# Kernel optimization log

Hardware: AMD Instinct MI355X
Metric: run time of the kernel (lower is better)

The kernel has to match this reference:

```python
import jax, jax.numpy as jnp
import numpy as np

N = 100000
E = 3200000
F_IN = 128
H = 64
B = 128


def _sage(x, edge_index, Wl, bl, Wr):
    # PyG SAGEConv (aggr='mean'): out = lin_l(mean_{j in N(i)} x_j) + lin_r(x_i)
    src, dst = edge_index[0], edge_index[1]
    msg = x[src]                                            # [E, F] gather
    agg = jax.ops.segment_sum(msg, dst, num_segments=x.shape[0])
    cnt = jax.ops.segment_sum(jnp.ones((edge_index.shape[1],), x.dtype), dst,
                              num_segments=x.shape[0])
    mean = agg / jnp.maximum(cnt, 1.0)[:, None]
    return mean @ Wl + bl + x @ Wr


def _encode(x, edge_index, batch, p1, p2, num_graphs):
    h = jax.nn.relu(_sage(x, edge_index, *p1))
    h = jax.nn.relu(_sage(h, edge_index, *p2))
    # global_mean_pool
    s = jax.ops.segment_sum(h, batch, num_segments=num_graphs)
    c = jax.ops.segment_sum(jnp.ones((h.shape[0],), h.dtype), batch,
                            num_segments=num_graphs)
    return s / jnp.maximum(c, 1.0)[:, None]


def setup_inputs() -> dict:
    key = jax.random.key(0)
    ks = jax.random.split(key, 20)
    inp = {
        "state_x": jax.random.normal(ks[0], (N, F_IN), dtype=jnp.float32),
        "state_edge_index": jax.random.randint(ks[1], (2, E), 0, N),
        "state_batch": jnp.sort(jax.random.randint(ks[2], (N,), 0, B)),
        "goal_x": jax.random.normal(ks[3], (N, F_IN), dtype=jnp.float32),
        "goal_edge_index": jax.random.randint(ks[4], (2, E), 0, N),
        "goal_batch": jnp.sort(jax.random.randint(ks[5], (N,), 0, B)),
        "depth": jax.random.uniform(ks[6], (B, 1), dtype=jnp.float32) * 20.0,
    }
    def lin(k, fin, fout):
        s = 1.0 / np.sqrt(fin)
        return jax.random.uniform(k, (fin, fout), minval=-s, maxval=s, dtype=jnp.float32)
    # SAGEConv params: Wl (neighbor, with bias), Wr (root, no bias)
    names = ["s1", "s2", "g1", "g2"]
    fins = [F_IN, H, F_IN, H]
    for i, (nm, fin) in enumerate(zip(names, fins)):
        inp[nm + "_Wl"] = lin(ks[7 + 3 * i], fin, H)
        inp[nm + "_bl"] = jnp.zeros((H,), jnp.float32)
        inp[nm + "_Wr"] = lin(ks[8 + 3 * i], fin, H)
    inp["mlp_W1"] = lin(ks[19], 2 * H + 1, H)
    inp["mlp_b1"] = jnp.zeros((H,), jnp.float32)
    inp["mlp_W2"] = lin(jax.random.fold_in(key, 99), H, 1)
    inp["mlp_b2"] = jnp.zeros((1,), jnp.float32)
    return inp


def reference(state_x, state_edge_index, state_batch,
              goal_x, goal_edge_index, goal_batch, depth,
              s1_Wl, s1_bl, s1_Wr, s2_Wl, s2_bl, s2_Wr,
              g1_Wl, g1_bl, g1_Wr, g2_Wl, g2_bl, g2_Wr,
              mlp_W1, mlp_b1, mlp_W2, mlp_b2):
    state_emb = _encode(state_x, state_edge_index, state_batch,
                        (s1_Wl, s1_bl, s1_Wr), (s2_Wl, s2_bl, s2_Wr), B)
    goal_emb = _encode(goal_x, goal_edge_index, goal_batch,
                       (g1_Wl, g1_bl, g1_Wr), (g2_Wl, g2_bl, g2_Wr), B)
    graph_emb = jnp.concatenate([state_emb, goal_emb], axis=1)   # [B, 2H]
    d_mean = depth.mean()
    d_std = depth.std()  # unbiased=False matches jnp default
    d = (depth - d_mean) / (d_std + 1e-6)
    features = jnp.concatenate([graph_emb, d], axis=1)           # [B, 2H+1]
    h = jax.nn.relu(features @ mlp_W1 + mlp_b1)
    out = h @ mlp_W2 + mlp_b2                                    # [B, 1]
    return out[:, 0]
```

## Files before the change

### kernel.cpp

```cpp
#include <hip/hip_runtime.h>
#include <hip/hip_bf16.h>
#include <hip/hip_fp16.h>


#define NB    128
#define EPB   16384
#define BWMAX 1024
#define PP    8
#define SRCB  17
#define SCAP  28672

typedef _Float16 v2h __attribute__((ext_vector_type(2)));
union U2H { unsigned int u; v2h h; __half2 hh; };

static __device__ __forceinline__ unsigned int pack2(float a, float b) {
    U2H t; t.hh = __floats2half2_rn(a, b); return t.u;
}
static __device__ __forceinline__ float dot2(unsigned int x, unsigned int w, float acc) {
    U2H xa, wa; xa.u = x; wa.u = w;
    return __builtin_amdgcn_fdot2(xa.h, wa.h, acc, false);
}


__global__ __launch_bounds__(256) void p1_hist(const int* __restrict__ dstS,
                                               const int* __restrict__ dstG,
                                               int* __restrict__ blkhist,
                                               int E, int bsh, int nblk) {
    const int g = blockIdx.x / nblk;
    const int blk = blockIdx.x % nblk;
    const int* __restrict__ dst = g ? dstG : dstS;
    __shared__ int h[NB];
    for (int i = threadIdx.x; i < NB; i += 256) h[i] = 0;
    __syncthreads();
    const int base = blk * EPB;
    for (int k = 0; k < EPB; k += 256) {
        const int e = base + k + threadIdx.x;
        if (e < E) atomicAdd(&h[dst[e] >> bsh], 1);
    }
    __syncthreads();
    for (int i = threadIdx.x; i < NB; i += 256)
        blkhist[((size_t)(g * nblk + blk)) * NB + i] = h[i];
}

__global__ __launch_bounds__(NB) void p1_scan(const int* __restrict__ blkhist,
                                              int* __restrict__ basem,
                                              int* __restrict__ bucket_base,
                                              int nblk) {
    __shared__ int lds[NB];
    const int g = blockIdx.x;
    const int* __restrict__ bh = blkhist + (size_t)g * nblk * NB;
    int* __restrict__ bm = basem + (size_t)g * nblk * NB;
    int* __restrict__ bb = bucket_base + (size_t)g * (NB + 1);
    const int b = threadIdx.x;
    int s = 0;
    int k = 0;
    for (; k + 8 <= nblk; k += 8) {
        int v[8];
        #pragma unroll
        for (int t = 0; t < 8; ++t) v[t] = bh[(size_t)(k + t) * NB + b];
        #pragma unroll
        for (int t = 0; t < 8; ++t) s += v[t];
    }
    for (; k < nblk; ++k) s += bh[(size_t)k * NB + b];
    lds[b] = s;
    __syncthreads();
    for (int off = 1; off < NB; off <<= 1) {
        int v = (b >= off) ? lds[b - off] : 0;
        __syncthreads();
        lds[b] += v;
        __syncthreads();
    }
    int run = lds[b] - s;
    bb[b] = run;
    if (b == NB - 1) bb[NB] = run + s;
    k = 0;
    for (; k + 8 <= nblk; k += 8) {
        int c[8];
        #pragma unroll
        for (int t = 0; t < 8; ++t) c[t] = bh[(size_t)(k + t) * NB + b];
        #pragma unroll
        for (int t = 0; t < 8; ++t) {
            bm[(size_t)(k + t) * NB + b] = run;
            run += c[t];
        }
    }
    for (; k < nblk; ++k) {
        const int c = bh[(size_t)k * NB + b];
        bm[(size_t)k * NB + b] = run;
        run += c;
    }
}

__global__ __launch_bounds__(256) void p1_scatter(const int* __restrict__ eiS,
                                                  const int* __restrict__ eiG,
                                                  const int* __restrict__ basem,
                                                  int* __restrict__ pairs,
                                                  int E, int bsh, int nblk) {
    const int g = blockIdx.x / nblk;
    const int blk = blockIdx.x % nblk;
    const int* __restrict__ src = g ? eiG : eiS;
    const int* __restrict__ dst = src + E;
    int* __restrict__ pr = pairs + (size_t)g * E;
    const int bwm = (1 << bsh) - 1;
    __shared__ int cur[NB];
    for (int i = threadIdx.x; i < NB; i += 256)
        cur[i] = basem[((size_t)(g * nblk + blk)) * NB + i];
    __syncthreads();
    const int base = blk * EPB;
    for (int k = 0; k < EPB; k += 256) {
        const int e = base + k + threadIdx.x;
        if (e < E) {
            const int d = dst[e];
            const int s = src[e];
            const int p = atomicAdd(&cur[d >> bsh], 1);
            pr[p] = s | ((d & bwm) << SRCB);
        }
    }
}

__global__ __launch_bounds__(512) void p2_sort(const int* __restrict__ pairs,
                                               const int* __restrict__ bucket_base,
                                               int* __restrict__ csr,
                                               int* __restrict__ row_start,
                                               int N, int E, int bsh) {
    __shared__ int stage[SCAP];
    __shared__ int cnt[BWMAX];
    __shared__ int off[BWMAX];
    __shared__ int ws[512];
    const int g = blockIdx.x / NB;
    const int b = blockIdx.x % NB;
    const int bw = 1 << bsh;
    const int lo = b * bw;
    int nn = N - lo;
    if (nn <= 0) return;
    if (nn > bw) nn = bw;
    const int* __restrict__ pr = pairs + (size_t)g * E;
    const int* __restrict__ bb = bucket_base + (size_t)g * (NB + 1);
    int* __restrict__ cs = csr + (size_t)g * E;
    int* __restrict__ rs = row_start + (size_t)g * (N + 1);
    const int tid = threadIdx.x;
    for (int i = tid; i < nn; i += 512) cnt[i] = 0;
    __syncthreads();
    const int e0 = bb[b];
    const int e1 = bb[b + 1];
    const int ne = e1 - e0;
    for (int e = e0 + tid; e < e1; e += 512)
        atomicAdd(&cnt[pr[e] >> SRCB], 1);
    __syncthreads();
    {
        const int i0 = 2 * tid, i1 = 2 * tid + 1;
        const int c0 = (i0 < nn) ? cnt[i0] : 0;
        const int c1 = (i1 < nn) ? cnt[i1] : 0;
        const int s = c0 + c1;
        ws[tid] = s;
        __syncthreads();
        for (int o = 1; o < 512; o <<= 1) {
            int v = (tid >= o) ? ws[tid - o] : 0;
            __syncthreads();
            ws[tid] += v;
            __syncthreads();
        }
        const int base = e0 + ws[tid] - s;
        if (i0 < nn) off[i0] = base;
        if (i1 < nn) off[i1] = base + c0;
    }
    __syncthreads();
    for (int i = tid; i < nn; i += 512) {
        rs[lo + i] = off[i];
        cnt[i] = off[i];
    }
    if (lo + nn == N && tid == 0) rs[N] = e1;
    __syncthreads();
    if (ne <= SCAP) {
        for (int e = e0 + tid; e < e1; e += 512) {
            const int v = pr[e];
            const int pos = atomicAdd(&cnt[v >> SRCB], 1);
            stage[pos - e0] = v & ((1 << SRCB) - 1);
        }
        __syncthreads();
        for (int i = tid; i < ne; i += 512) cs[e0 + i] = stage[i];
    } else {
        for (int e = e0 + tid; e < e1; e += 512) {
            const int v = pr[e];
            const int pos = atomicAdd(&cnt[v >> SRCB], 1);
            cs[pos] = v & ((1 << SRCB) - 1);
        }
    }
}

template <int K>
__global__ __launch_bounds__(512) void gemm_fused(const float* __restrict__ x,
                                                  const float* __restrict__ Wl,
                                                  const float* __restrict__ Wr,
                                                  __hip_bfloat16* __restrict__ Y,
                                                  __hip_bfloat16* __restrict__ R, int n) {
    constexpr int KC = 64;
    constexpr int ROWS = 64;
    __shared__ uint4 ldsW4[(KC / 4) * 64];
    __shared__ unsigned int ldsXu[ROWS * (KC / 2)];
    const int tid = threadIdx.x;
    const int lane = tid & 63;
    const int wid = tid >> 6;
    const int rbase = blockIdx.x * ROWS;

    float accY[8], accR[8];
    #pragma unroll
    for (int r = 0; r < 8; ++r) { accY[r] = 0.f; accR[r] = 0.f; }

    for (int k0 = 0; k0 < K; k0 += KC) {
        __syncthreads();
        for (int i = tid; i < (KC / 4) * 64; i += 512) {
            const int gp = i >> 6;
            const int c = i & 63;
            const int ka = k0 + gp * 4;
            const float wl0 = Wl[(size_t)ka * 64 + c],       wr0 = Wr[(size_t)ka * 64 + c];
            const float wl1 = Wl[(size_t)(ka + 1) * 64 + c], wr1 = Wr[(size_t)(ka + 1) * 64 + c];
            const float wl2 = Wl[(size_t)(ka + 2) * 64 + c], wr2 = Wr[(size_t)(ka + 2) * 64 + c];
            const float wl3 = Wl[(size_t)(ka + 3) * 64 + c], wr3 = Wr[(size_t)(ka + 3) * 64 + c];
            ldsW4[i] = make_uint4(pack2(wl0, wl1), pack2(wr0, wr1),
                                  pack2(wl2, wl3), pack2(wr2, wr3));
        }
        {
            constexpr int F4R = KC / 4;
            for (int i = tid; i < ROWS * F4R; i += 512) {
                const int rr = i / F4R;
                const int cc = i % F4R;
                int row = rbase + rr;
                if (row > n - 1) row = n - 1;
                const float4 xv = *(const float4*)(x + (size_t)row * K + k0 + cc * 4);
                ldsXu[rr * (KC / 2) + cc * 2 + 0] = pack2(xv.x, xv.y);
                ldsXu[rr * (KC / 2) + cc * 2 + 1] = pack2(xv.z, xv.w);
            }
        }
        __syncthreads();
        const int rw = wid * 8;
        #pragma unroll 2
        for (int k8 = 0; k8 < KC / 8; ++k8) {
            const uint4 w0 = ldsW4[(k8 * 2 + 0) * 64 + lane];
            const uint4 w1 = ldsW4[(k8 * 2 + 1) * 64 + lane];
            #pragma unroll
            for (int r = 0; r < 8; ++r) {
                const uint4 xq = *(const uint4*)(&ldsXu[(rw + r) * (KC / 2) + k8 * 4]);
                float yv = accY[r];
                float zv = accR[r];
                yv = dot2(xq.x, w0.x, yv);
                zv = dot2(xq.x, w0.y, zv);
                yv = dot2(xq.y, w0.z, yv);
                zv = dot2(xq.y, w0.w, zv);
                yv = dot2(xq.z, w1.x, yv);
                zv = dot2(xq.z, w1.y, zv);
                yv = dot2(xq.w, w1.z, yv);
                zv = dot2(xq.w, w1.w, zv);
                accY[r] = yv;
                accR[r] = zv;
            }
        }
    }
    #pragma unroll
    for (int r = 0; r < 8; ++r) {
        const int row = rbase + wid * 8 + r;
        if (row < n) {
            Y[(size_t)row * 64 + lane] = __float2bfloat16(accY[r]);
            R[(size_t)row * 64 + lane] = __float2bfloat16(accR[r]);
        }
    }
}

__global__ __launch_bounds__(256) void agg_fused(const __hip_bfloat16* __restrict__ Y,
                                                 const __hip_bfloat16* __restrict__ R,
                                                 const float* __restrict__ bl,
                                                 const int* __restrict__ csr,
                                                 const int* __restrict__ row_start,
                                                 float* __restrict__ H, int n) {
    const int wid = threadIdx.x >> 6;
    const int lane = threadIdx.x & 63;
    const int i = blockIdx.x * 4 + wid;
    if (i >= n) return;
    const int r0 = __builtin_amdgcn_readfirstlane(row_start[i]);
    const int r1 = __builtin_amdgcn_readfirstlane(row_start[i + 1]);
    float a[32];
    #pragma unroll
    for (int t = 0; t < 32; ++t) a[t] = 0.f;
    int e = r0;
    for (; e + 32 <= r1; e += 32) {
        #pragma unroll
        for (int t = 0; t < 32; ++t)
            a[t] += __bfloat162float(Y[(size_t)csr[e + t] * 64 + lane]);
    }
    for (; e + 8 <= r1; e += 8) {
        #pragma unroll
        for (int t = 0; t < 8; ++t)
            a[t] += __bfloat162float(Y[(size_t)csr[e + t] * 64 + lane]);
    }
    for (; e < r1; ++e) a[0] += __bfloat162float(Y[(size_t)csr[e] * 64 + lane]);
    float acc = 0.f;
    #pragma unroll
    for (int t = 0; t < 32; ++t) acc += a[t];
    const int c = r1 - r0;
    const float sc = (c > 0) ? (1.0f / (float)c) : 1.0f;
    const float v = acc * sc + bl[lane] + __bfloat162float(R[(size_t)i * 64 + lane]);
    H[(size_t)i * 64 + lane] = fmaxf(v, 0.0f);
}

__global__ __launch_bounds__(256) void pool_part(const float* __restrict__ H,
                                                 const int* __restrict__ batch,
                                                 float* __restrict__ parts,
                                                 int* __restrict__ pcnt, int n) {
    const int b = blockIdx.x / PP;
    const int p = blockIdx.x % PP;
    int lo = 0, hi = n;
    while (lo < hi) { int m = (lo + hi) >> 1; if (batch[m] < b) lo = m + 1; else hi = m; }
    const int beg = lo;
    hi = n;
    while (lo < hi) { int m = (lo + hi) >> 1; if (batch[m] < b + 1) lo = m + 1; else hi = m; }
    const int end = lo;
    const int len = end - beg;
    const int chunk = (len + PP - 1) / PP;
    const int s0 = beg + p * chunk;
    int s1 = s0 + chunk; if (s1 > end) s1 = end;

    const int wid = threadIdx.x >> 6;
    const int lane = threadIdx.x & 63;
    float acc = 0.f;
    for (int i = s0 + wid; i < s1; i += 4)
        acc += H[(size_t)i * 64 + lane];
    __shared__ float part[4][64];
    part[wid][lane] = acc;
    __syncthreads();
    if (wid == 0) {
        const float s = (part[0][lane] + part[1][lane]) + (part[2][lane] + part[3][lane]);
        parts[(size_t)(b * PP + p) * 64 + lane] = s;
        if (lane == 0 && p == 0) pcnt[b] = len;
    }
}

__global__ __launch_bounds__(64) void final_mlp(const float* __restrict__ partsS,
                                                const int* __restrict__ cntS,
                                                const float* __restrict__ partsG,
                                                const int* __restrict__ cntG,
                                                const float* __restrict__ depth,
                                                const float* __restrict__ W1,
                                                const float* __restrict__ b1,
                                                const float* __restrict__ W2,
                                                const float* __restrict__ b2,
                                                float* __restrict__ out, int Bn) {
    const int b = blockIdx.x;
    const int j = threadIdx.x;
    float dsum = 0.f;
    for (int i = j; i < Bn; i += 64) dsum += depth[i];
    #pragma unroll
    for (int o = 32; o > 0; o >>= 1) dsum += __shfl_xor(dsum, o);
    const float mean = dsum / (float)Bn;
    float dvar = 0.f;
    for (int i = j; i < Bn; i += 64) { const float t = depth[i] - mean; dvar = fmaf(t, t, dvar); }
    #pragma unroll
    for (int o = 32; o > 0; o >>= 1) dvar += __shfl_xor(dvar, o);
    const float stdv = sqrtf(dvar / (float)Bn);
    const float dn = (depth[b] - mean) / (stdv + 1e-6f);

    __shared__ float f[129];
    {
        float s = 0.f, g = 0.f;
        #pragma unroll
        for (int p = 0; p < PP; ++p) {
            s += partsS[(size_t)(b * PP + p) * 64 + j];
            g += partsG[(size_t)(b * PP + p) * 64 + j];
        }
        int cs = cntS[b]; if (cs < 1) cs = 1;
        int cg = cntG[b]; if (cg < 1) cg = 1;
        f[j] = s / (float)cs;
        f[64 + j] = g / (float)cg;
        if (j == 0) f[128] = dn;
    }
    __syncthreads();
    float acc = b1[j];
    #pragma unroll 8
    for (int k = 0; k < 129; ++k)
        acc = fmaf(f[k], W1[(size_t)k * 64 + j], acc);
    float o = fmaxf(acc, 0.0f) * W2[j];
    #pragma unroll
    for (int of = 32; of > 0; of >>= 1) o += __shfl_xor(o, of);
    if (j == 0) out[b] = o + b2[0];
}

extern "C" void kernel_launch(void* const* d_in, const int* in_sizes, int n_in,
                              void* d_out, int out_size, void* d_ws, size_t ws_size,
                              hipStream_t stream) {
    const float* state_x     = (const float*)d_in[0];
    const int*   state_ei    = (const int*)d_in[1];
    const int*   state_batch = (const int*)d_in[2];
    const float* goal_x      = (const float*)d_in[3];
    const int*   goal_ei     = (const int*)d_in[4];
    const int*   goal_batch  = (const int*)d_in[5];
    const float* depth       = (const float*)d_in[6];
    const float* s1_Wl = (const float*)d_in[7];
    const float* s1_bl = (const float*)d_in[8];
    const float* s1_Wr = (const float*)d_in[9];
    const float* s2_Wl = (const float*)d_in[10];
    const float* s2_bl = (const float*)d_in[11];
    const float* s2_Wr = (const float*)d_in[12];
    const float* g1_Wl = (const float*)d_in[13];
    const float* g1_bl = (const float*)d_in[14];
    const float* g1_Wr = (const float*)d_in[15];
    const float* g2_Wl = (const float*)d_in[16];
    const float* g2_bl = (const float*)d_in[17];
    const float* g2_Wr = (const float*)d_in[18];
    const float* mlp_W1 = (const float*)d_in[19];
    const float* mlp_b1 = (const float*)d_in[20];
    const float* mlp_W2 = (const float*)d_in[21];
    const float* mlp_b2 = (const float*)d_in[22];

    const int N  = in_sizes[0] / 128;
    const int E  = in_sizes[1] / 2;
    const int Bn = in_sizes[6];
    const int nblk = (E + EPB - 1) / EPB;
    int bsh = 0;
    while (((size_t)NB << bsh) < (size_t)N) ++bsh;

    char* w = (char*)d_ws;
    auto alloc = [&](size_t bytes) {
        char* p = w;
        w += (bytes + 255) & ~(size_t)255;
        return p;
    };
    char*  bufYraw     = alloc((size_t)N * 64 * sizeof(float));
    char*  bufRraw     = alloc((size_t)N * 64 * sizeof(__hip_bfloat16));
    float* bufH        = (float*)alloc((size_t)N * 64 * sizeof(float));
    int*   csr         = (int*)alloc((size_t)2 * E * sizeof(int));
    int*   row_start   = (int*)alloc((size_t)2 * (N + 1) * sizeof(int));
    int*   blkhist     = (int*)alloc((size_t)2 * nblk * NB * sizeof(int));
    int*   basem       = (int*)alloc((size_t)2 * nblk * NB * sizeof(int));
    int*   bucket_base = (int*)alloc((size_t)2 * (NB + 1) * sizeof(int));
    float* partsS      = (float*)alloc((size_t)Bn * PP * 64 * sizeof(float));
    float* partsG      = (float*)alloc((size_t)Bn * PP * 64 * sizeof(float));
    int*   cntS        = (int*)alloc((size_t)Bn * sizeof(int));
    int*   cntG        = (int*)alloc((size_t)Bn * sizeof(int));
    __hip_bfloat16* bufY = (__hip_bfloat16*)bufYraw;
    __hip_bfloat16* bufR = (__hip_bfloat16*)bufRraw;
    int*   pairs       = (int*)bufYraw;
    const size_t need = (size_t)(w - (char*)d_ws);
    const bool pairs_fit = (size_t)2 * E * sizeof(int) <= (size_t)N * 64 * sizeof(float);
    if (need > ws_size || (1 << bsh) > BWMAX || !pairs_fit || N > (1 << SRCB)) {
        hipMemsetAsync(d_out, 0, (size_t)out_size * sizeof(float), stream);
        return;
    }

    p1_hist<<<2 * nblk, 256, 0, stream>>>(state_ei + E, goal_ei + E, blkhist, E, bsh, nblk);
    p1_scan<<<2, NB, 0, stream>>>(blkhist, basem, bucket_base, nblk);
    p1_scatter<<<2 * nblk, 256, 0, stream>>>(state_ei, goal_ei, basem, pairs, E, bsh, nblk);
    p2_sort<<<2 * NB, 512, 0, stream>>>(pairs, bucket_base, csr, row_start, N, E, bsh);

    const int g64 = (N + 63) / 64;
    const int g4  = (N + 3) / 4;
    const int* csrS = csr;
    const int* csrG = csr + E;
    const int* rsS  = row_start;
    const int* rsG  = row_start + (N + 1);

    gemm_fused<128><<<g64, 512, 0, stream>>>(state_x, s1_Wl, s1_Wr, bufY, bufR, N);
    agg_fused<<<g4, 256, 0, stream>>>(bufY, bufR, s1_bl, csrS, rsS, bufH, N);
    gemm_fused<64><<<g64, 512, 0, stream>>>(bufH, s2_Wl, s2_Wr, bufY, bufR, N);
    agg_fused<<<g4, 256, 0, stream>>>(bufY, bufR, s2_bl, csrS, rsS, bufH, N);
    pool_part<<<Bn * PP, 256, 0, stream>>>(bufH, state_batch, partsS, cntS, N);

    gemm_fused<128><<<g64, 512, 0, stream>>>(goal_x, g1_Wl, g1_Wr, bufY, bufR, N);
    agg_fused<<<g4, 256, 0, stream>>>(bufY, bufR, g1_bl, csrG, rsG, bufH, N);
    gemm_fused<64><<<g64, 512, 0, stream>>>(bufH, g2_Wl, g2_Wr, bufY, bufR, N);
    agg_fused<<<g4, 256, 0, stream>>>(bufY, bufR, g2_bl, csrG, rsG, bufH, N);
    pool_part<<<Bn * PP, 256, 0, stream>>>(bufH, goal_batch, partsG, cntG, N);

    final_mlp<<<Bn, 64, 0, stream>>>(partsS, cntS, partsG, cntG, depth,
                                     mlp_W1, mlp_b1, mlp_W2, mlp_b2, (float*)d_out, Bn);
}
```

Before: 577.9 us.

## Batch state and goal encoders into single launches per stage

Merges the state and goal graph pipelines so each GEMM, aggregation and pooling stage runs once over both graphs, with the block index choosing which graph to process. Buffers are doubled to hold both graphs at once. The aggregation kernel also moves to 1024-thread blocks covering 16 nodes each. The aim is to halve the launch count and give each launch more blocks to fill the GPU and hide tail effects, at the cost of a larger workspace and possible occupancy changes from the bigger blocks.

```diff
diff --git a/kernel.cpp b/kernel.cpp
--- a/kernel.cpp
+++ b/kernel.cpp
@@ -189,19 +189,30 @@
 }
 
 template <int K>
-__global__ __launch_bounds__(512) void gemm_fused(const float* __restrict__ x,
-                                                  const float* __restrict__ Wl,
-                                                  const float* __restrict__ Wr,
+__global__ __launch_bounds__(512) void gemm_fused(const float* __restrict__ xS,
+                                                  const float* __restrict__ xG,
+                                                  const float* __restrict__ WlS,
+                                                  const float* __restrict__ WrS,
+                                                  const float* __restrict__ WlG,
+                                                  const float* __restrict__ WrG,
                                                   __hip_bfloat16* __restrict__ Y,
-                                                  __hip_bfloat16* __restrict__ R, int n) {
+                                                  __hip_bfloat16* __restrict__ R,
+                                                  int n, int nbg) {
     constexpr int KC = 64;
     constexpr int ROWS = 64;
     __shared__ uint4 ldsW4[(KC / 4) * 64];
     __shared__ unsigned int ldsXu[ROWS * (KC / 2)];
+    const int g = (blockIdx.x >= nbg) ? 1 : 0;
+    const int blk = blockIdx.x - g * nbg;
+    const float* __restrict__ x  = g ? xG : xS;
+    const float* __restrict__ Wl = g ? WlG : WlS;
+    const float* __restrict__ Wr = g ? WrG : WrS;
+    __hip_bfloat16* __restrict__ Yp = Y + (size_t)g * n * 64;
+    __hip_bfloat16* __restrict__ Rp = R + (size_t)g * n * 64;
     const int tid = threadIdx.x;
     const int lane = tid & 63;
     const int wid = tid >> 6;
-    const int rbase = blockIdx.x * ROWS;
+    const int rbase = blk * ROWS;
 
     float accY[8], accR[8];
     #pragma unroll
@@ -260,24 +271,35 @@
     for (int r = 0; r < 8; ++r) {
         const int row = rbase + wid * 8 + r;
         if (row < n) {
-            Y[(size_t)row * 64 + lane] = __float2bfloat16(accY[r]);
-            R[(size_t)row * 64 + lane] = __float2bfloat16(accR[r]);
-        }
-    }
-}
-
-__global__ __launch_bounds__(256) void agg_fused(const __hip_bfloat16* __restrict__ Y,
-                                                 const __hip_bfloat16* __restrict__ R,
-                                                 const float* __restrict__ bl,
-                                                 const int* __restrict__ csr,
-                                                 const int* __restrict__ row_start,
-                                                 float* __restrict__ H, int n) {
+            Yp[(size_t)row * 64 + lane] = __float2bfloat16(accY[r]);
+            Rp[(size_t)row * 64 + lane] = __float2bfloat16(accR[r]);
+        }
+    }
+}
+
+__global__ __launch_bounds__(1024) void agg_fused(const __hip_bfloat16* __restrict__ Y,
+                                                  const __hip_bfloat16* __restrict__ R,
+                                                  const float* __restrict__ blS,
+                                                  const float* __restrict__ blG,
+                                                  const int* __restrict__ csr,
+                                                  const int* __restrict__ row_start,
+                                                  float* __restrict__ H,
+                                                  int n, int E, int nbg) {
+    const int g = (blockIdx.x >= nbg) ? 1 : 0;
+    const int blk = blockIdx.x - g * nbg;
     const int wid = threadIdx.x >> 6;
     const int lane = threadIdx.x & 63;
-    const int i = blockIdx.x * 4 + wid;
+    const int i = blk * 16 + wid;
     if (i >= n) return;
-    const int r0 = __builtin_amdgcn_readfirstlane(row_start[i]);
-    const int r1 = __builtin_amdgcn_readfirstlane(row_start[i + 1]);
+    const int* __restrict__ rs = row_start + (size_t)g * (n + 1);
+    const int* __restrict__ cs = csr + (size_t)g * E;
+    const __hip_bfloat16* __restrict__ Yp = Y + (size_t)g * n * 64;
+    const __hip_bfloat16* __restrict__ Rp = R + (size_t)g * n * 64;
+    const float* __restrict__ bl = g ? blG : blS;
+    float* __restrict__ Hp = H + (size_t)g * n * 64;
+
+    const int r0 = __builtin_amdgcn_readfirstlane(rs[i]);
+    const int r1 = __builtin_amdgcn_readfirstlane(rs[i + 1]);
     float a[32];
     #pragma unroll
     for (int t = 0; t < 32; ++t) a[t] = 0.f;
@@ -285,29 +307,40 @@
     for (; e + 32 <= r1; e += 32) {
         #pragma unroll
         for (int t = 0; t < 32; ++t)
-            a[t] += __bfloat162float(Y[(size_t)csr[e + t] * 64 + lane]);
+            a[t] += __bfloat162float(Yp[(size_t)cs[e + t] * 64 + lane]);
     }
     for (; e + 8 <= r1; e += 8) {
         #pragma unroll
         for (int t = 0; t < 8; ++t)
-            a[t] += __bfloat162float(Y[(size_t)csr[e + t] * 64 + lane]);
-    }
-    for (; e < r1; ++e) a[0] += __bfloat162float(Y[(size_t)csr[e] * 64 + lane]);
+            a[t] += __bfloat162float(Yp[(size_t)cs[e + t] * 64 + lane]);
+    }
+    for (; e < r1; ++e) a[0] += __bfloat162float(Yp[(size_t)cs[e] * 64 + lane]);
     float acc = 0.f;
     #pragma unroll
     for (int t = 0; t < 32; ++t) acc += a[t];
     const int c = r1 - r0;
     const float sc = (c > 0) ? (1.0f / (float)c) : 1.0f;
-    const float v = acc * sc + bl[lane] + __bfloat162float(R[(size_t)i * 64 + lane]);
-    H[(size_t)i * 64 + lane] = fmaxf(v, 0.0f);
+    const float v = acc * sc + bl[lane] + __bfloat162float(Rp[(size_t)i * 64 + lane]);
+    Hp[(size_t)i * 64 + lane] = fmaxf(v, 0.0f);
 }
 
 __global__ __launch_bounds__(256) void pool_part(const float* __restrict__ H,
-                                                 const int* __restrict__ batch,
-                                                 float* __restrict__ parts,
-                                                 int* __restrict__ pcnt, int n) {
-    const int b = blockIdx.x / PP;
-    const int p = blockIdx.x % PP;
+                                                 const int* __restrict__ batchS,
+                                                 const int* __restrict__ batchG,
+                                                 float* __restrict__ partsS,
+                                                 float* __restrict__ partsG,
+                                                 int* __restrict__ cntS,
+                                                 int* __restrict__ cntG,
+                                                 int n, int nbg) {
+    const int g = (blockIdx.x >= nbg) ? 1 : 0;
+    const int blk = blockIdx.x - g * nbg;
+    const int b = blk / PP;
+    const int p = blk % PP;
+    const int* __restrict__ batch = g ? batchG : batchS;
+    const float* __restrict__ Hp = H + (size_t)g * n * 64;
+    float* __restrict__ parts = g ? partsG : partsS;
+    int* __restrict__ pcnt = g ? cntG : cntS;
+
     int lo = 0, hi = n;
     while (lo < hi) { int m = (lo + hi) >> 1; if (batch[m] < b) lo = m + 1; else hi = m; }
     const int beg = lo;
@@ -323,7 +356,7 @@
     const int lane = threadIdx.x & 63;
     float acc = 0.f;
     for (int i = s0 + wid; i < s1; i += 4)
-        acc += H[(size_t)i * 64 + lane];
+        acc += Hp[(size_t)i * 64 + lane];
     __shared__ float part[4][64];
     part[wid][lane] = acc;
     __syncthreads();
@@ -423,9 +456,9 @@
         w += (bytes + 255) & ~(size_t)255;
         return p;
     };
-    char*  bufYraw     = alloc((size_t)N * 64 * sizeof(float));
-    char*  bufRraw     = alloc((size_t)N * 64 * sizeof(__hip_bfloat16));
-    float* bufH        = (float*)alloc((size_t)N * 64 * sizeof(float));
+    char*  bufYraw     = alloc((size_t)2 * N * 64 * sizeof(__hip_bfloat16));
+    char*  bufRraw     = alloc((size_t)2 * N * 64 * sizeof(__hip_bfloat16));
+    float* bufH        = (float*)alloc((size_t)2 * N * 64 * sizeof(float));
     int*   csr         = (int*)alloc((size_t)2 * E * sizeof(int));
     int*   row_start   = (int*)alloc((size_t)2 * (N + 1) * sizeof(int));
     int*   blkhist     = (int*)alloc((size_t)2 * nblk * NB * sizeof(int));
@@ -439,7 +472,7 @@
     __hip_bfloat16* bufR = (__hip_bfloat16*)bufRraw;
     int*   pairs       = (int*)bufYraw;
     const size_t need = (size_t)(w - (char*)d_ws);
-    const bool pairs_fit = (size_t)2 * E * sizeof(int) <= (size_t)N * 64 * sizeof(float);
+    const bool pairs_fit = (size_t)2 * E * sizeof(int) <= (size_t)2 * N * 64 * sizeof(__hip_bfloat16);
     if (need > ws_size || (1 << bsh) > BWMAX || !pairs_fit || N > (1 << SRCB)) {
         hipMemsetAsync(d_out, 0, (size_t)out_size * sizeof(float), stream);
         return;
@@ -450,24 +483,22 @@
     p1_scatter<<<2 * nblk, 256, 0, stream>>>(state_ei, goal_ei, basem, pairs, E, bsh, nblk);
     p2_sort<<<2 * NB, 512, 0, stream>>>(pairs, bucket_base, csr, row_start, N, E, bsh);
 
-    const int g64 = (N + 63) / 64;
-    const int g4  = (N + 3) / 4;
-    const int* csrS = csr;
-    const int* csrG = csr + E;
-    const int* rsS  = row_start;
-    const int* rsG  = row_start + (N + 1);
-
-    gemm_fused<128><<<g64, 512, 0, stream>>>(state_x, s1_Wl, s1_Wr, bufY, bufR, N);
-    agg_fused<<<g4, 256, 0, stream>>>(bufY, bufR, s1_bl, csrS, rsS, bufH, N);
-    gemm_fused<64><<<g64, 512, 0, stream>>>(bufH, s2_Wl, s2_Wr, bufY, bufR, N);
-    agg_fused<<<g4, 256, 0, stream>>>(bufY, bufR, s2_bl, csrS, rsS, bufH, N);
-    pool_part<<<Bn * PP, 256, 0, stream>>>(bufH, state_batch, partsS, cntS, N);
-
-    gemm_fused<128><<<g64, 512, 0, stream>>>(goal_x, g1_Wl, g1_Wr, bufY, bufR, N);
-    agg_fused<<<g4, 256, 0, stream>>>(bufY, bufR, g1_bl, csrG, rsG, bufH, N);
-    gemm_fused<64><<<g64, 512, 0, stream>>>(bufH, g2_Wl, g2_Wr, bufY, bufR, N);
-    agg_fused<<<g4, 256, 0, stream>>>(bufY, bufR, g2_bl, csrG, rsG, bufH, N);
-    pool_part<<<Bn * PP, 256, 0, stream>>>(bufH, goal_batch, partsG, cntG, N);
+    const int g64  = (N + 63) / 64;
+    const int g16  = (N + 15) / 16;
+    const int gpp  = Bn * PP;
+
+    gemm_fused<128><<<2 * g64, 512, 0, stream>>>(state_x, goal_x,
+                                                 s1_Wl, s1_Wr, g1_Wl, g1_Wr,
+                                                 bufY, bufR, N, g64);
+    agg_fused<<<2 * g16, 1024, 0, stream>>>(bufY, bufR, s1_bl, g1_bl,
+                                            csr, row_start, bufH, N, E, g16);
+    gemm_fused<64><<<2 * g64, 512, 0, stream>>>(bufH, bufH + (size_t)N * 64,
+                                                s2_Wl, s2_Wr, g2_Wl, g2_Wr,
+                                                bufY, bufR, N, g64);
+    agg_fused<<<2 * g16, 1024, 0, stream>>>(bufY, bufR, s2_bl, g2_bl,
+                                            csr, row_start, bufH, N, E, g16);
+    pool_part<<<2 * gpp, 256, 0, stream>>>(bufH, state_batch, goal_batch,
+                                           partsS, partsG, cntS, cntG, N, gpp);
 
     final_mlp<<<Bn, 64, 0, stream>>>(partsS, cntS, partsG, cntG, depth,
                                      mlp_W1, mlp_b1, mlp_W2, mlp_b2, (float*)d_out, Bn);
```

After: 712.1 us. +23.2%, slower.
